# Performance work log

Hardware: AMD Instinct MI355X
Metric: run time of the kernel (lower is better)

Reference implementation:

```python
import jax, jax.numpy as jnp
import numpy as np

B, T, C, H = 2, 2048, 1024, 16
D = C // H  # head_dim = 64


def setup_inputs() -> dict:
    key = jax.random.key(0)
    ks = jax.random.split(key, 5)
    s = 1.0 / np.sqrt(C)
    return {
        "x": jax.random.normal(ks[0], (B, T, C), jnp.float32),
        "Wq": jax.random.normal(ks[1], (C, C), jnp.float32) * s,
        "bq": jnp.zeros((C,), jnp.float32),
        "Wk": jax.random.normal(ks[2], (C, C), jnp.float32) * s,
        "bk": jnp.zeros((C,), jnp.float32),
        "Wv": jax.random.normal(ks[3], (C, C), jnp.float32) * s,
        "bv": jnp.zeros((C,), jnp.float32),
        "Wo": jax.random.normal(ks[4], (C, C), jnp.float32) * s,
        "bo": jnp.zeros((C,), jnp.float32),
    }


def reference(x, Wq, bq, Wk, bk, Wv, bv, Wo, bo):
    Bx, Tx, Cx = x.shape
    # torch Linear: y = x @ W.T + b
    q = (x @ Wq.T + bq).reshape(Bx, Tx, H, D).transpose(0, 2, 1, 3)  # [B,H,T,D]
    k = (x @ Wk.T + bk).reshape(Bx, Tx, H, D).transpose(0, 2, 1, 3)
    v = (x @ Wv.T + bv).reshape(Bx, Tx, H, D).transpose(0, 2, 1, 3)
    att = jnp.einsum("bhqd,bhkd->bhqk", q, k) / np.sqrt(D).astype(np.float32)
    mask = jnp.tril(jnp.ones((Tx, Tx), bool))  # causal mask [T,T]
    att = jnp.where(mask, att, -jnp.inf)
    att = jax.nn.softmax(att, axis=-1)
    out = jnp.einsum("bhqk,bhkd->bhqd", att, v)
    out = out.transpose(0, 2, 1, 3).reshape(Bx, Tx, Cx)
    return out @ Wo.T + bo
```

## Files before the change

### kernel.cpp

```cpp
#include <hip/hip_runtime.h>
#include <hip/hip_bf16.h>

#define B_ 2
#define T_ 2048
#define C_ 1024
#define H_ 16
#define D_ 64

typedef unsigned short u16;
typedef __bf16 bf16x8 __attribute__((ext_vector_type(8)));
typedef float floatx4 __attribute__((ext_vector_type(4)));

__device__ __forceinline__ float bf2f(u16 u) {
  union { unsigned int i; float f; } x; x.i = ((unsigned int)u) << 16; return x.f;
}
__device__ __forceinline__ u16 f2bf(float f) {
  union { float f; unsigned int i; } x; x.f = f;
  unsigned int r = x.i + 0x7fffu + ((x.i >> 16) & 1u);
  return (u16)(r >> 16);
}

__device__ __forceinline__ void gld16(void* lds, const void* g) {
  __builtin_amdgcn_global_load_lds(
      (const __attribute__((address_space(1))) unsigned int*)g,
      (__attribute__((address_space(3))) unsigned int*)lds, 16, 0, 0);
}

#define NXF4 1048576
#define NWF4 262144

__global__ __launch_bounds__(256) void cvt_all(
    const float* __restrict__ x,  const float* __restrict__ Wq,
    const float* __restrict__ Wk, const float* __restrict__ Wv,
    const float* __restrict__ Wo, u16* __restrict__ dst_base)
{
  const int i = blockIdx.x * 256 + threadIdx.x;
  const float* src; size_t off;
  if (i < NXF4)               { src = x;  off = i; }
  else if (i < NXF4 + NWF4)   { src = Wq; off = i - NXF4; }
  else if (i < NXF4 + 2*NWF4) { src = Wk; off = i - (NXF4 + NWF4); }
  else if (i < NXF4 + 3*NWF4) { src = Wv; off = i - (NXF4 + 2*NWF4); }
  else                        { src = Wo; off = i - (NXF4 + 3*NWF4); }
  float4 f = ((const float4*)src)[off];
  ushort4 o;
  o.x = f2bf(f.x); o.y = f2bf(f.y); o.z = f2bf(f.z); o.w = f2bf(f.w);
  ((ushort4*)dst_base)[i] = o;
}

#define QSCALE 0.1803368801111f

__global__ __launch_bounds__(256) void gemm128(
    const u16* __restrict__ X, const u16* __restrict__ Wb,
    const float* __restrict__ b0, const float* __restrict__ b1,
    const float* __restrict__ b2,
    u16* __restrict__ Yq, u16* __restrict__ Yk, u16* __restrict__ Yv,
    float* __restrict__ Yf, int qkv)
{
  const int K = C_, N = C_;
  __shared__ __align__(16) u16 As[128 * 32];
  __shared__ __align__(16) u16 Bs[128 * 32];

  const int tid  = threadIdx.x;
  const int wv   = tid >> 6;
  const int lane = tid & 63;
  const int mcol = lane & 15;
  const int quad = lane >> 4;
  const int wr = wv >> 1, wc = wv & 1;
  const int m0 = blockIdx.x * 128;
  const int n0 = blockIdx.y * 128;
  const int z  = qkv ? (int)blockIdx.z : 0;

  const u16* W = qkv ? (Wb + (size_t)z * C_ * C_) : Wb;
  const float* bias = qkv ? (z == 0 ? b0 : z == 1 ? b1 : b2) : b0;

  const int srow = tid >> 2;
  const int scol = (tid & 3) * 8;
  const u16* xp0 = X + (size_t)(m0 + srow) * K + scol;
  const u16* xp1 = xp0 + (size_t)64 * K;
  const u16* wp0 = W + (size_t)(n0 + srow) * K + scol;
  const u16* wp1 = wp0 + (size_t)64 * K;

  floatx4 acc[4][4] = {};

  for (int k0 = 0; k0 < K; k0 += 32) {
    gld16(&As[tid * 8],        xp0 + k0);
    gld16(&As[2048 + tid * 8], xp1 + k0);
    gld16(&Bs[tid * 8],        wp0 + k0);
    gld16(&Bs[2048 + tid * 8], wp1 + k0);
    __syncthreads();

    bf16x8 a[4], b[4];
#pragma unroll
    for (int rf = 0; rf < 4; ++rf)
      a[rf] = *(const bf16x8*)&As[(wr * 64 + rf * 16 + mcol) * 32 + quad * 8];
#pragma unroll
    for (int cf = 0; cf < 4; ++cf)
      b[cf] = *(const bf16x8*)&Bs[(wc * 64 + cf * 16 + mcol) * 32 + quad * 8];
#pragma unroll
    for (int rf = 0; rf < 4; ++rf)
#pragma unroll
      for (int cf = 0; cf < 4; ++cf)
        acc[rf][cf] = __builtin_amdgcn_mfma_f32_16x16x32_bf16(
            a[rf], b[cf], acc[rf][cf], 0, 0, 0);
    __syncthreads();
  }

#pragma unroll
  for (int cf = 0; cf < 4; ++cf) {
    const int n = n0 + wc * 64 + cf * 16 + mcol;
    const float bv = bias[n];
#pragma unroll
    for (int rf = 0; rf < 4; ++rf) {
#pragma unroll
      for (int r = 0; r < 4; ++r) {
        const int m = m0 + wr * 64 + rf * 16 + quad * 4 + r;
        const float v = acc[rf][cf][r] + bv;
        if (!qkv) {
          Yf[(size_t)m * N + n] = v;
        } else {
          const int bb = m >> 11, t = m & (T_ - 1);
          const int h = n >> 6, d = n & (D_ - 1);
          if (z == 0)
            Yq[(((size_t)bb * H_ + h) * T_ + t) * D_ + d] = f2bf(v * QSCALE);
          else if (z == 1)
            Yk[(((size_t)bb * H_ + h) * T_ + t) * D_ + d] = f2bf(v);
          else
            Yv[(((size_t)bb * H_ + h) * D_ + d) * T_ + t] = f2bf(v);
        }
      }
    }
  }
}

__global__ __launch_bounds__(256) void attn_flash(
    const u16* __restrict__ Q, const u16* __restrict__ K,
    const u16* __restrict__ Vg, u16* __restrict__ O)
{
  __shared__ __align__(16) u16 Ks[64 * 64];
  __shared__ __align__(16) u16 Vt[80 * 64];
  __shared__ __align__(16) u16 Ps[4][16 * 72];

  const int tid  = threadIdx.x;
  const int wv   = tid >> 6;
  const int lane = tid & 63;
  const int mcol = lane & 15;
  const int quad = lane >> 4;

  const int bh = blockIdx.x & 31;
  const int pp = blockIdx.x >> 5;
  const size_t base = (size_t)bh * T_ * D_;
  const int b = bh >> 4, h = bh & (H_ - 1);

  for (int idx = tid; idx < 16 * 64; idx += 256)
    Vt[64 * 64 + idx] = (idx < 64) ? (u16)0x3F80 : (u16)0;

  const int srow = lane >> 3;
  const int sg   = (lane & 7) ^ srow;
  const int c0 = wv * 2, c1 = wv * 2 + 1;

  const int sl0 = (quad ^ (mcol & 7)) * 8;

  const int h3 = mcol >> 3, lo = mcol & 7;
  u16* psw = &Ps[wv][0];
  int colsw[4];
#pragma unroll
  for (int nt = 0; nt < 4; ++nt)
    colsw[nt] = (((nt * 2 + h3) ^ quad) * 8) + lo;
  const int g0 = quad ^ (mcol >> 2);

  for (int half = 0; half < 2; ++half) {
    const int iq = half ? (31 - pp) : pp;

    const u16* qg = Q + base + (size_t)(iq * 64 + wv * 16 + mcol) * D_ + quad * 8;
    const bf16x8 qf0 = *(const bf16x8*)qg;
    const bf16x8 qf1 = *(const bf16x8*)(qg + 32);

    floatx4 oacc[5] = {};

    for (int j = 0; j <= iq; ++j) {
      __syncthreads();
      gld16(&Ks[c0 * 512 + lane * 8],
            K + base + (size_t)(j * 64 + c0 * 8 + srow) * D_ + sg * 8);
      gld16(&Ks[c1 * 512 + lane * 8],
            K + base + (size_t)(j * 64 + c1 * 8 + srow) * D_ + sg * 8);
      gld16(&Vt[c0 * 512 + lane * 8],
            Vg + (size_t)bh * D_ * T_ + (size_t)(c0 * 8 + srow) * T_ + j * 64 + sg * 8);
      gld16(&Vt[c1 * 512 + lane * 8],
            Vg + (size_t)bh * D_ * T_ + (size_t)(c1 * 8 + srow) * T_ + j * 64 + sg * 8);
      __syncthreads();

      floatx4 sacc[4] = {};
#pragma unroll
      for (int nt = 0; nt < 4; ++nt) {
        const u16* kr = &Ks[(nt * 16 + mcol) * 64];
        bf16x8 kb0 = *(const bf16x8*)&kr[sl0];
        bf16x8 kb1 = *(const bf16x8*)&kr[sl0 ^ 32];
        sacc[nt] = __builtin_amdgcn_mfma_f32_16x16x32_bf16(qf0, kb0, sacc[nt], 0, 0, 0);
        sacc[nt] = __builtin_amdgcn_mfma_f32_16x16x32_bf16(qf1, kb1, sacc[nt], 0, 0, 0);
      }

      if (j == iq) {
#pragma unroll
        for (int nt = 0; nt < 4; ++nt) {
          const int col = nt * 16 + mcol;
#pragma unroll
          for (int r = 0; r < 4; ++r)
            if (col > wv * 16 + quad * 4 + r) sacc[nt][r] = -1e30f;
        }
      }

#pragma unroll
      for (int nt = 0; nt < 4; ++nt)
#pragma unroll
        for (int r = 0; r < 4; ++r) {
          const float p = exp2f(sacc[nt][r]);
          psw[(quad * 4 + r) * 72 + colsw[nt]] =
              (u16)((__float_as_uint(p) + 0x8000u) >> 16);
        }

      __builtin_amdgcn_wave_barrier();

      bf16x8 pa0 = *(const bf16x8*)&psw[mcol * 72 + g0 * 8];
      bf16x8 pa1 = *(const bf16x8*)&psw[mcol * 72 + g0 * 8 + 32];
#pragma unroll
      for (int dt = 0; dt < 5; ++dt) {
        const u16* vr = &Vt[(dt * 16 + mcol) * 64];
        bf16x8 vb0 = *(const bf16x8*)&vr[sl0];
        bf16x8 vb1 = *(const bf16x8*)&vr[sl0 ^ 32];
        oacc[dt] = __builtin_amdgcn_mfma_f32_16x16x32_bf16(pa0, vb0, oacc[dt], 0, 0, 0);
        oacc[dt] = __builtin_amdgcn_mfma_f32_16x16x32_bf16(pa1, vb1, oacc[dt], 0, 0, 0);
      }
    }

    float invl[4];
#pragma unroll
    for (int r = 0; r < 4; ++r)
      invl[r] = 1.f / __shfl(oacc[4][r], lane & 48);
#pragma unroll
    for (int dt = 0; dt < 4; ++dt) {
      const int c = h * D_ + dt * 16 + mcol;
#pragma unroll
      for (int r = 0; r < 4; ++r) {
        const int t = iq * 64 + wv * 16 + quad * 4 + r;
        O[((size_t)b * T_ + t) * C_ + c] = f2bf(oacc[dt][r] * invl[r]);
      }
    }
  }
}

extern "C" void kernel_launch(void* const* d_in, const int* in_sizes, int n_in,
                              void* d_out, int out_size, void* d_ws, size_t ws_size,
                              hipStream_t stream) {
  const float* x  = (const float*)d_in[0];
  const float* Wq = (const float*)d_in[1];
  const float* bq = (const float*)d_in[2];
  const float* Wk = (const float*)d_in[3];
  const float* bk = (const float*)d_in[4];
  const float* Wv = (const float*)d_in[5];
  const float* bv = (const float*)d_in[6];
  const float* Wo = (const float*)d_in[7];
  const float* bo = (const float*)d_in[8];
  float* out = (float*)d_out;

  const size_t NX = (size_t)B_ * T_ * C_;
  const size_t NW = (size_t)C_ * C_;

  u16* xb  = (u16*)d_ws;
  u16* wqb = xb  + NX;
  u16* wkb = wqb + NW;
  u16* wvb = wkb + NW;
  u16* wob = wvb + NW;
  u16* q   = wob + NW;
  u16* k   = q   + NX;
  u16* v   = k   + NX;
  u16* ctx = v   + NX;

  cvt_all<<<dim3((NXF4 + 4 * NWF4) / 256), 256, 0, stream>>>(x, Wq, Wk, Wv, Wo, xb);

  gemm128<<<dim3(32, 8, 3), 256, 0, stream>>>(
      xb, wqb, bq, bk, bv, q, k, v, nullptr, 1);

  attn_flash<<<dim3(512), 256, 0, stream>>>(q, k, v, ctx);

  gemm128<<<dim3(32, 8, 1), 256, 0, stream>>>(
      ctx, wob, bo, nullptr, nullptr, nullptr, nullptr, nullptr, out, 0);
}
```

Before: 200.6 us.

## Stage V-transpose epilogue through LDS and split output GEMM into narrower tiles

The QKV projection GEMM now writes the transposed V output through a swizzled shared-memory staging buffer, so the global stores along T become coalesced 16-byte writes instead of scattered 2-byte ones. The output projection becomes its own kernel with 128x64 tiles, doubling the grid to 512 blocks so more of the GPU's compute units have work. The cost is extra LDS for the staging buffer, which may lower occupancy in the QKV kernel, and less operand reuse per block in the output GEMM.

Result: no change. 202.1 us (+0.8%).

```diff
diff --git a/kernel.cpp b/kernel.cpp
--- a/kernel.cpp
+++ b/kernel.cpp
@@ -49,16 +49,16 @@
 
 #define QSCALE 0.1803368801111f
 
-__global__ __launch_bounds__(256) void gemm128(
+__global__ __launch_bounds__(256) void gemm_qkv(
     const u16* __restrict__ X, const u16* __restrict__ Wb,
     const float* __restrict__ b0, const float* __restrict__ b1,
     const float* __restrict__ b2,
-    u16* __restrict__ Yq, u16* __restrict__ Yk, u16* __restrict__ Yv,
-    float* __restrict__ Yf, int qkv)
+    u16* __restrict__ Yq, u16* __restrict__ Yk, u16* __restrict__ Yv)
 {
-  const int K = C_, N = C_;
+  const int K = C_;
   __shared__ __align__(16) u16 As[128 * 32];
   __shared__ __align__(16) u16 Bs[128 * 32];
+  __shared__ __align__(16) u16 Es[64 * 128];
 
   const int tid  = threadIdx.x;
   const int wv   = tid >> 6;
@@ -68,10 +68,10 @@
   const int wr = wv >> 1, wc = wv & 1;
   const int m0 = blockIdx.x * 128;
   const int n0 = blockIdx.y * 128;
-  const int z  = qkv ? (int)blockIdx.z : 0;
-
-  const u16* W = qkv ? (Wb + (size_t)z * C_ * C_) : Wb;
-  const float* bias = qkv ? (z == 0 ? b0 : z == 1 ? b1 : b2) : b0;
+  const int z  = blockIdx.z;
+
+  const u16* W = Wb + (size_t)z * C_ * C_;
+  const float* bias = (z == 0 ? b0 : z == 1 ? b1 : b2);
 
   const int srow = tid >> 2;
   const int scol = (tid & 3) * 8;
@@ -105,28 +105,121 @@
     __syncthreads();
   }
 
-#pragma unroll
-  for (int cf = 0; cf < 4; ++cf) {
-    const int n = n0 + wc * 64 + cf * 16 + mcol;
+  if (z == 2) {
+#pragma unroll
+    for (int p = 0; p < 2; ++p) {
+      __syncthreads();
+      if (wc == p) {
+#pragma unroll
+        for (int cf = 0; cf < 4; ++cf) {
+          const int rn = cf * 16 + mcol;
+          const float bv = b2[n0 + p * 64 + rn];
+#pragma unroll
+          for (int rf = 0; rf < 4; ++rf) {
+            const int gm = wr * 8 + rf * 2 + (quad >> 1);
+            const int slot = gm ^ (rn & 7);
+            ushort4 pk;
+            pk.x = f2bf(acc[rf][cf][0] + bv);
+            pk.y = f2bf(acc[rf][cf][1] + bv);
+            pk.z = f2bf(acc[rf][cf][2] + bv);
+            pk.w = f2bf(acc[rf][cf][3] + bv);
+            *(ushort4*)&Es[rn * 128 + slot * 8 + (quad & 1) * 4] = pk;
+          }
+        }
+      }
+      __syncthreads();
+      const int c = tid & 15;
+      const int bb = m0 >> 11;
+      const int t0 = (m0 & (T_ - 1)) + c * 8;
+#pragma unroll
+      for (int i = 0; i < 4; ++i) {
+        const int rn = (tid >> 4) + i * 16;
+        const int slot = c ^ (rn & 7);
+        const uint4 val = *(const uint4*)&Es[rn * 128 + slot * 8];
+        const int n = n0 + p * 64 + rn;
+        const int h = n >> 6, d = n & (D_ - 1);
+        *(uint4*)&Yv[(((size_t)bb * H_ + h) * D_ + d) * T_ + t0] = val;
+      }
+    }
+  } else {
+#pragma unroll
+    for (int cf = 0; cf < 4; ++cf) {
+      const int n = n0 + wc * 64 + cf * 16 + mcol;
+      const float bv = bias[n];
+      const int h = n >> 6, d = n & (D_ - 1);
+#pragma unroll
+      for (int rf = 0; rf < 4; ++rf) {
+#pragma unroll
+        for (int r = 0; r < 4; ++r) {
+          const int m = m0 + wr * 64 + rf * 16 + quad * 4 + r;
+          const int bb = m >> 11, t = m & (T_ - 1);
+          const float v = acc[rf][cf][r] + bv;
+          const size_t idx = (((size_t)bb * H_ + h) * T_ + t) * D_ + d;
+          if (z == 0) Yq[idx] = f2bf(v * QSCALE);
+          else        Yk[idx] = f2bf(v);
+        }
+      }
+    }
+  }
+}
+
+__global__ __launch_bounds__(256) void gemm_out(
+    const u16* __restrict__ X, const u16* __restrict__ W,
+    const float* __restrict__ bias, float* __restrict__ Yf)
+{
+  const int K = C_, N = C_;
+  __shared__ __align__(16) u16 As[128 * 32];
+  __shared__ __align__(16) u16 Bs[64 * 32];
+
+  const int tid  = threadIdx.x;
+  const int wv   = tid >> 6;
+  const int lane = tid & 63;
+  const int mcol = lane & 15;
+  const int quad = lane >> 4;
+  const int wr = wv >> 1, wc = wv & 1;
+  const int m0 = blockIdx.x * 128;
+  const int n0 = blockIdx.y * 64;
+
+  const int srow = tid >> 2;
+  const int scol = (tid & 3) * 8;
+  const u16* xp0 = X + (size_t)(m0 + srow) * K + scol;
+  const u16* xp1 = xp0 + (size_t)64 * K;
+  const u16* wp  = W + (size_t)(n0 + srow) * K + scol;
+
+  floatx4 acc[4][2] = {};
+
+  for (int k0 = 0; k0 < K; k0 += 32) {
+    gld16(&As[tid * 8],        xp0 + k0);
+    gld16(&As[2048 + tid * 8], xp1 + k0);
+    gld16(&Bs[tid * 8],        wp + k0);
+    __syncthreads();
+
+    bf16x8 a[4], b[2];
+#pragma unroll
+    for (int rf = 0; rf < 4; ++rf)
+      a[rf] = *(const bf16x8*)&As[(wr * 64 + rf * 16 + mcol) * 32 + quad * 8];
+#pragma unroll
+    for (int cf = 0; cf < 2; ++cf)
+      b[cf] = *(const bf16x8*)&Bs[(wc * 32 + cf * 16 + mcol) * 32 + quad * 8];
+#pragma unroll
+    for (int rf = 0; rf < 4; ++rf)
+#pragma unroll
+      for (int cf = 0; cf < 2; ++cf)
+        acc[rf][cf] = __builtin_amdgcn_mfma_f32_16x16x32_bf16(
+            a[rf], b[cf], acc[rf][cf], 0, 0, 0);
+    __syncthreads();
+  }
+
+#pragma unroll
+  for (int cf = 0; cf < 2; ++cf) {
+    const int n = n0 + wc * 32 + cf * 16 + mcol;
     const float bv = bias[n];
 #pragma unroll
     for (int rf = 0; rf < 4; ++rf) {
 #pragma unroll
       for (int r = 0; r < 4; ++r) {
         const int m = m0 + wr * 64 + rf * 16 + quad * 4 + r;
-        const float v = acc[rf][cf][r] + bv;
-        if (!qkv) {
-          Yf[(size_t)m * N + n] = v;
-        } else {
-          const int bb = m >> 11, t = m & (T_ - 1);
-          const int h = n >> 6, d = n & (D_ - 1);
-          if (z == 0)
-            Yq[(((size_t)bb * H_ + h) * T_ + t) * D_ + d] = f2bf(v * QSCALE);
-          else if (z == 1)
-            Yk[(((size_t)bb * H_ + h) * T_ + t) * D_ + d] = f2bf(v);
-          else
-            Yv[(((size_t)bb * H_ + h) * D_ + d) * T_ + t] = f2bf(v);
-        }
+        Yf[(size_t)m * N + n] = acc[rf][cf][r] + bv;
       }
     }
   }
@@ -157,7 +250,6 @@
   const int srow = lane >> 3;
   const int sg   = (lane & 7) ^ srow;
   const int c0 = wv * 2, c1 = wv * 2 + 1;
-
   const int sl0 = (quad ^ (mcol & 7)) * 8;
 
   const int h3 = mcol >> 3, lo = mcol & 7;
@@ -277,11 +369,9 @@
 
   cvt_all<<<dim3((NXF4 + 4 * NWF4) / 256), 256, 0, stream>>>(x, Wq, Wk, Wv, Wo, xb);
 
-  gemm128<<<dim3(32, 8, 3), 256, 0, stream>>>(
-      xb, wqb, bq, bk, bv, q, k, v, nullptr, 1);
+  gemm_qkv<<<dim3(32, 8, 3), 256, 0, stream>>>(xb, wqb, bq, bk, bv, q, k, v);
 
   attn_flash<<<dim3(512), 256, 0, stream>>>(q, k, v, ctx);
 
-  gemm128<<<dim3(32, 8, 1), 256, 0, stream>>>(
-      ctx, wob, bo, nullptr, nullptr, nullptr, nullptr, nullptr, out, 0);
-}
+  gemm_out<<<dim3(32, 16), 256, 0, stream>>>(ctx, wob, bo, out);
+}
```
